# Kernel optimization log

Hardware: AMD Instinct MI355X
Metric: run time of the kernel (lower is better)

## Reference

```python
import jax, jax.numpy as jnp
import numpy as np

B, IN_DIM, OUT_DIM, N = 8, 128, 128, 256
BN_EPS = 1e-5


def setup_inputs() -> dict:
    key = jax.random.key(0)
    ks = jax.random.split(key, 6)
    A = jax.random.normal(ks[0], (B, IN_DIM, N), dtype=jnp.float32)
    ini_p = float(np.sqrt(3.0 / OUT_DIM / IN_DIM))
    ini_qk = float(np.sqrt(1.0 / OUT_DIM / IN_DIM))
    P1 = jax.random.uniform(ks[1], (OUT_DIM, IN_DIM), minval=-ini_p, maxval=ini_p, dtype=jnp.float32)
    P2 = jax.random.uniform(ks[2], (OUT_DIM, IN_DIM), minval=-ini_p, maxval=ini_p, dtype=jnp.float32)
    q = jax.random.uniform(ks[3], (OUT_DIM, IN_DIM), minval=-ini_qk, maxval=ini_qk, dtype=jnp.float32)
    k = jax.random.uniform(ks[4], (OUT_DIM, IN_DIM), minval=-ini_qk, maxval=ini_qk, dtype=jnp.float32)
    gamma = jnp.ones((OUT_DIM,), dtype=jnp.float32)
    beta = jnp.zeros((OUT_DIM,), dtype=jnp.float32)
    return {"A": A, "P1": P1, "P2": P2, "q": q, "k": k,
            "gamma": gamma, "beta": beta,
            "permutation_size1": N, "BATCH_SIZE": B}


def reference(A, P1, P2, q, k, gamma, beta, permutation_size1, BATCH_SIZE):
    # A: [B, in_dim, n]; params [out_dim, in_dim]
    A1 = jnp.einsum('oi,bin->bon', P1, A)            # [B, C, n]
    Q = jnp.einsum('oi,bin->bon', q, A)              # [B, C, n]
    K = jnp.einsum('oi,bin->bon', k, A)              # [B, C, n]
    # Rank-1 outer product per (b, c): Alpha[b,c,i,j] = Q[b,c,i] * K[b,c,j]
    Alpha = Q[..., :, None] * K[..., None, :]        # [B, C, n, n]
    row_norm = jnp.linalg.norm(Alpha, axis=3, keepdims=True)  # [B, C, n, 1]
    Alpha_norm = jnp.abs(Alpha) / row_norm
    V = jnp.einsum('oi,bin->bon', P2, A)             # [B, C, n]
    Y = jnp.einsum('bcij,bcj->bci', Alpha_norm, V)   # [B, C, n]
    out = A1 + V + 0.1 * Y
    out = jax.nn.relu(out)
    # BatchNorm1d (training mode): normalize per channel over (B, n)
    mean = out.mean(axis=(0, 2), keepdims=True)
    var = out.var(axis=(0, 2), keepdims=True)
    out = (out - mean) * jax.lax.rsqrt(var + BN_EPS)
    out = out * gamma[None, :, None] + beta[None, :, None]
    return out
```

## Files before the change

kernel.cpp:

```cpp
#include <hip/hip_runtime.h>
#include <math.h>

#define BB   8
#define IND  128
#define OUTD 128
#define NN   256
#define BN_EPS 1e-5f

__global__ __launch_bounds__(256) void layer1dpe_fused(
    const float* __restrict__ A,
    const float* __restrict__ P1,
    const float* __restrict__ P2,
    const float* __restrict__ kw,
    const float* __restrict__ gamma,
    const float* __restrict__ beta,
    float* __restrict__ out)
{
    const int c = blockIdx.x;
    const int t = threadIdx.x;

    __shared__ float w1[IND], w2[IND], wk[IND];
    if (t < IND) {
        w1[t] = P1[c * IND + t];
        w2[t] = P2[c * IND + t];
        wk[t] = kw[c * IND + t];
    }
    __syncthreads();

    float a1[BB], vv[BB], kv[BB];
    #pragma unroll
    for (int b = 0; b < BB; ++b) { a1[b] = 0.f; vv[b] = 0.f; kv[b] = 0.f; }

    #pragma unroll 4
    for (int i = 0; i < IND; ++i) {
        const float wa = w1[i];
        const float wb = w2[i];
        const float wc = wk[i];
        #pragma unroll
        for (int b = 0; b < BB; ++b) {
            const float a = A[(b * IND + i) * NN + t];
            a1[b] = fmaf(wa, a, a1[b]);
            vv[b] = fmaf(wb, a, vv[b]);
            kv[b] = fmaf(wc, a, kv[b]);
        }
    }

    __shared__ float red[2][4];
    const int wave = t >> 6;
    const int lane = t & 63;

    float pre[BB];
    float bnsum = 0.f, bnsq = 0.f;

    #pragma unroll
    for (int b = 0; b < BB; ++b) {
        float s2 = kv[b] * kv[b];
        float sv = fabsf(kv[b]) * vv[b];
        #pragma unroll
        for (int off = 32; off >= 1; off >>= 1) {
            s2 += __shfl_xor(s2, off, 64);
            sv += __shfl_xor(sv, off, 64);
        }
        if (lane == 0) { red[0][wave] = s2; red[1][wave] = sv; }
        __syncthreads();
        const float S2 = red[0][0] + red[0][1] + red[0][2] + red[0][3];
        const float SV = red[1][0] + red[1][1] + red[1][2] + red[1][3];
        __syncthreads();

        const float y = SV / sqrtf(S2);
        float p = a1[b] + vv[b] + 0.1f * y;
        p = fmaxf(p, 0.f);
        pre[b] = p;
        bnsum += p;
        bnsq  += p * p;
    }

    #pragma unroll
    for (int off = 32; off >= 1; off >>= 1) {
        bnsum += __shfl_xor(bnsum, off, 64);
        bnsq  += __shfl_xor(bnsq,  off, 64);
    }
    if (lane == 0) { red[0][wave] = bnsum; red[1][wave] = bnsq; }
    __syncthreads();
    const float tsum = red[0][0] + red[0][1] + red[0][2] + red[0][3];
    const float tsq  = red[1][0] + red[1][1] + red[1][2] + red[1][3];

    const float inv  = 1.f / (float)(BB * NN);
    const float mean = tsum * inv;
    const float var  = tsq * inv - mean * mean;
    const float scale = gamma[c] * rsqrtf(var + BN_EPS);
    const float shift = beta[c] - mean * scale;

    #pragma unroll
    for (int b = 0; b < BB; ++b) {
        out[(b * OUTD + c) * NN + t] = fmaf(pre[b], scale, shift);
    }
}

extern "C" void kernel_launch(void* const* d_in, const int* in_sizes, int n_in,
                              void* d_out, int out_size, void* d_ws, size_t ws_size,
                              hipStream_t stream) {
    const float* A     = (const float*)d_in[0];
    const float* P1    = (const float*)d_in[1];
    const float* P2    = (const float*)d_in[2];
    const float* kw    = (const float*)d_in[4];
    const float* gamma = (const float*)d_in[5];
    const float* beta  = (const float*)d_in[6];
    float* out = (float*)d_out;

    layer1dpe_fused<<<OUTD, 256, 0, stream>>>(A, P1, P2, kw, gamma, beta, out);
}
```

Measured before the change: 87.98 us.

## Remap threads to one wave per batch with float4 loads and wave-local reductions

The block becomes 64x8 threads. Each wave handles one batch and each lane covers 4 consecutive n positions, reading them with float4 loads and writing them with float4 stores. The per-batch row-norm reduction now stays inside a single wave, which removes the 16 block-wide barriers the old per-batch loop needed; only the final BatchNorm reduction goes through shared memory. Each thread keeps 12 accumulators instead of 24 and the block doubles in size, so register pressure drops and more waves are active, at the cost of a different reduction order.

```diff
diff --git a/kernel.cpp b/kernel.cpp
--- a/kernel.cpp
+++ b/kernel.cpp
@@ -5,9 +5,10 @@
 #define IND  128
 #define OUTD 128
 #define NN   256
+#define NQ   64
 #define BN_EPS 1e-5f
 
-__global__ __launch_bounds__(256) void layer1dpe_fused(
+__global__ __launch_bounds__(512) void layer1dpe_fused(
     const float* __restrict__ A,
     const float* __restrict__ P1,
     const float* __restrict__ P2,
@@ -16,63 +17,60 @@
     const float* __restrict__ beta,
     float* __restrict__ out)
 {
-    const int c = blockIdx.x;
-    const int t = threadIdx.x;
+    const int c    = blockIdx.x;
+    const int x    = threadIdx.x;
+    const int b    = threadIdx.y;
 
     __shared__ float w1[IND], w2[IND], wk[IND];
-    if (t < IND) {
-        w1[t] = P1[c * IND + t];
-        w2[t] = P2[c * IND + t];
-        wk[t] = kw[c * IND + t];
+    {
+        const int tid = b * 64 + x;
+        if (tid < IND) {
+            w1[tid] = P1[c * IND + tid];
+            w2[tid] = P2[c * IND + tid];
+            wk[tid] = kw[c * IND + tid];
+        }
     }
     __syncthreads();
 
-    float a1[BB], vv[BB], kv[BB];
+    const float4* __restrict__ A4 = (const float4*)A;
+    float a1[4], vv[4], kv[4];
     #pragma unroll
-    for (int b = 0; b < BB; ++b) { a1[b] = 0.f; vv[b] = 0.f; kv[b] = 0.f; }
+    for (int j = 0; j < 4; ++j) { a1[j] = 0.f; vv[j] = 0.f; kv[j] = 0.f; }
 
-    #pragma unroll 4
+    #pragma unroll 8
     for (int i = 0; i < IND; ++i) {
-        const float wa = w1[i];
-        const float wb = w2[i];
-        const float wc = wk[i];
-        #pragma unroll
-        for (int b = 0; b < BB; ++b) {
-            const float a = A[(b * IND + i) * NN + t];
-            a1[b] = fmaf(wa, a, a1[b]);
-            vv[b] = fmaf(wb, a, vv[b]);
-            kv[b] = fmaf(wc, a, kv[b]);
-        }
+        const float4 a = A4[(b * IND + i) * NQ + x];
+        const float wa = w1[i], wb = w2[i], wc = wk[i];
+        a1[0] = fmaf(wa, a.x, a1[0]); a1[1] = fmaf(wa, a.y, a1[1]);
+        a1[2] = fmaf(wa, a.z, a1[2]); a1[3] = fmaf(wa, a.w, a1[3]);
+        vv[0] = fmaf(wb, a.x, vv[0]); vv[1] = fmaf(wb, a.y, vv[1]);
+        vv[2] = fmaf(wb, a.z, vv[2]); vv[3] = fmaf(wb, a.w, vv[3]);
+        kv[0] = fmaf(wc, a.x, kv[0]); kv[1] = fmaf(wc, a.y, kv[1]);
+        kv[2] = fmaf(wc, a.z, kv[2]); kv[3] = fmaf(wc, a.w, kv[3]);
     }
 
-    __shared__ float red[2][4];
-    const int wave = t >> 6;
-    const int lane = t & 63;
+    float s2 = 0.f, sv = 0.f;
+    #pragma unroll
+    for (int j = 0; j < 4; ++j) {
+        s2 = fmaf(kv[j], kv[j], s2);
+        sv = fmaf(fabsf(kv[j]), vv[j], sv);
+    }
+    #pragma unroll
+    for (int off = 32; off >= 1; off >>= 1) {
+        s2 += __shfl_xor(s2, off, 64);
+        sv += __shfl_xor(sv, off, 64);
+    }
+    const float y = sv / sqrtf(s2);
 
-    float pre[BB];
+    float p[4];
     float bnsum = 0.f, bnsq = 0.f;
-
     #pragma unroll
-    for (int b = 0; b < BB; ++b) {
-        float s2 = kv[b] * kv[b];
-        float sv = fabsf(kv[b]) * vv[b];
-        #pragma unroll
-        for (int off = 32; off >= 1; off >>= 1) {
-            s2 += __shfl_xor(s2, off, 64);
-            sv += __shfl_xor(sv, off, 64);
-        }
-        if (lane == 0) { red[0][wave] = s2; red[1][wave] = sv; }
-        __syncthreads();
-        const float S2 = red[0][0] + red[0][1] + red[0][2] + red[0][3];
-        const float SV = red[1][0] + red[1][1] + red[1][2] + red[1][3];
-        __syncthreads();
-
-        const float y = SV / sqrtf(S2);
-        float p = a1[b] + vv[b] + 0.1f * y;
-        p = fmaxf(p, 0.f);
-        pre[b] = p;
-        bnsum += p;
-        bnsq  += p * p;
+    for (int j = 0; j < 4; ++j) {
+        float t = a1[j] + vv[j] + 0.1f * y;
+        t = fmaxf(t, 0.f);
+        p[j] = t;
+        bnsum += t;
+        bnsq  = fmaf(t, t, bnsq);
     }
 
     #pragma unroll
@@ -80,21 +78,23 @@
         bnsum += __shfl_xor(bnsum, off, 64);
         bnsq  += __shfl_xor(bnsq,  off, 64);
     }
-    if (lane == 0) { red[0][wave] = bnsum; red[1][wave] = bnsq; }
+    __shared__ float red[BB][2];
+    if (x == 0) { red[b][0] = bnsum; red[b][1] = bnsq; }
     __syncthreads();
-    const float tsum = red[0][0] + red[0][1] + red[0][2] + red[0][3];
-    const float tsq  = red[1][0] + red[1][1] + red[1][2] + red[1][3];
+    float tsum = 0.f, tsq = 0.f;
+    #pragma unroll
+    for (int w = 0; w < BB; ++w) { tsum += red[w][0]; tsq += red[w][1]; }
 
-    const float inv  = 1.f / (float)(BB * NN);
-    const float mean = tsum * inv;
-    const float var  = tsq * inv - mean * mean;
+    const float inv   = 1.f / (float)(BB * NN);
+    const float mean  = tsum * inv;
+    const float var   = tsq * inv - mean * mean;
     const float scale = gamma[c] * rsqrtf(var + BN_EPS);
     const float shift = beta[c] - mean * scale;
 
-    #pragma unroll
-    for (int b = 0; b < BB; ++b) {
-        out[(b * OUTD + c) * NN + t] = fmaf(pre[b], scale, shift);
-    }
+    float4* __restrict__ out4 = (float4*)out;
+    out4[(b * OUTD + c) * NQ + x] = make_float4(
+        fmaf(p[0], scale, shift), fmaf(p[1], scale, shift),
+        fmaf(p[2], scale, shift), fmaf(p[3], scale, shift));
 }
 
 extern "C" void kernel_launch(void* const* d_in, const int* in_sizes, int n_in,
@@ -108,5 +108,6 @@
     const float* beta  = (const float*)d_in[6];
     float* out = (float*)d_out;
 
-    layer1dpe_fused<<<OUTD, 256, 0, stream>>>(A, P1, P2, kw, gamma, beta, out);
+    dim3 block(64, 8);
+    layer1dpe_fused<<<OUTD, block, 0, stream>>>(A, P1, P2, kw, gamma, beta, out);
 }
```

After: 102.9 us. 16.9% more time.
